# Kernel optimization log

Hardware: AMD Instinct MI355X
Metric: run time of the kernel (lower is better)

## Reference

```python
import jax, jax.numpy as jnp
import numpy as np
from jax import lax

# Model dims (mamba_ssm defaults: d_state=16, d_conv=4, expand=2, dt_rank=ceil(d_model/16))
V = 16384       # vocab_size
D = 1024        # embedding_dim / d_model
C_CLS = 128     # num_CLS_classes
D_INNER = 2 * D # expand * d_model = 2048
N = 16          # d_state
K = 4           # d_conv
DT_RANK = (D + 15) // 16  # 64
B, L = 4, 512


def setup_inputs() -> dict:
    key = jax.random.key(0)
    ks = jax.random.split(key, 12)
    s = 0.02
    tokens = jax.random.randint(ks[0], (B, L), 0, V, dtype=jnp.int64)
    embedding = jax.random.normal(ks[1], (V, D), jnp.float32) * s
    in_proj_w = jax.random.normal(ks[2], (2 * D_INNER, D), jnp.float32) * s
    conv_w = jax.random.normal(ks[3], (D_INNER, 1, K), jnp.float32) * 0.1
    conv_b = jnp.zeros((D_INNER,), jnp.float32)
    x_proj_w = jax.random.normal(ks[4], (DT_RANK + 2 * N, D_INNER), jnp.float32) * s
    dt_proj_w = jax.random.normal(ks[5], (D_INNER, DT_RANK), jnp.float32) * s
    dt_proj_b = jax.random.uniform(ks[6], (D_INNER,), jnp.float32, -4.0, -2.0)  # softplus -> small dt
    A_log = jnp.log(jnp.broadcast_to(jnp.arange(1, N + 1, dtype=jnp.float32), (D_INNER, N)))
    D_param = jnp.ones((D_INNER,), jnp.float32)
    out_proj_w = jax.random.normal(ks[7], (D, D_INNER), jnp.float32) * s
    recon_w = jax.random.normal(ks[8], (V, D), jnp.float32) * s
    cls_w = jax.random.normal(ks[9], (C_CLS, D), jnp.float32) * s
    return dict(tokens=tokens, embedding=embedding, in_proj_w=in_proj_w,
                conv_w=conv_w, conv_b=conv_b, x_proj_w=x_proj_w,
                dt_proj_w=dt_proj_w, dt_proj_b=dt_proj_b, A_log=A_log,
                D_param=D_param, out_proj_w=out_proj_w, recon_w=recon_w, cls_w=cls_w)


def _mamba(h, in_proj_w, conv_w, conv_b, x_proj_w, dt_proj_w, dt_proj_b, A_log, D_param, out_proj_w):
    # h: (B, L, D)
    xz = jnp.einsum('bld,ed->ble', h, in_proj_w)          # (B, L, 2*D_INNER)
    x, z = jnp.split(xz, 2, axis=-1)                      # each (B, L, D_INNER)
    # causal depthwise conv1d along L
    xt = jnp.swapaxes(x, 1, 2)                            # (B, D_INNER, L)
    xt = lax.conv_general_dilated(xt, conv_w, window_strides=(1,),
                                  padding=[(K - 1, 0)],
                                  feature_group_count=D_INNER,
                                  dimension_numbers=('NCH', 'OIH', 'NCH'))
    xt = xt + conv_b[None, :, None]
    x = jax.nn.silu(jnp.swapaxes(xt, 1, 2))               # (B, L, D_INNER)
    # input-dependent dt, B, C
    x_dbl = jnp.einsum('bld,ed->ble', x, x_proj_w)        # (B, L, DT_RANK+2N)
    dt, Bm, Cm = jnp.split(x_dbl, [DT_RANK, DT_RANK + N], axis=-1)
    delta = jax.nn.softplus(jnp.einsum('blr,dr->bld', dt, dt_proj_w) + dt_proj_b)  # (B,L,D_INNER)
    A = -jnp.exp(A_log)                                   # (D_INNER, N)
    dA = jnp.exp(delta[..., None] * A)                    # (B,L,D_INNER,N)
    dBx = delta[..., None] * Bm[:, :, None, :] * x[..., None]  # (B,L,D_INNER,N)
    # selective scan over time (sequential recurrence)
    dA_t = jnp.swapaxes(dA, 0, 1)                         # (L,B,D_INNER,N)
    dBx_t = jnp.swapaxes(dBx, 0, 1)
    C_t = jnp.swapaxes(Cm, 0, 1)                          # (L,B,N)
    def step(hc, inp):
        a, bx, c = inp
        hc = a * hc + bx                                  # (B,D_INNER,N)
        y = jnp.einsum('bdn,bn->bd', hc, c)
        return hc, y
    h0 = jnp.zeros((x.shape[0], D_INNER, N), x.dtype)
    _, ys = lax.scan(step, h0, (dA_t, dBx_t, C_t))
    y = jnp.swapaxes(ys, 0, 1) + x * D_param              # (B,L,D_INNER)
    y = y * jax.nn.silu(z)
    return jnp.einsum('ble,de->bld', y, out_proj_w)       # (B,L,D)


def reference(tokens, embedding, in_proj_w, conv_w, conv_b, x_proj_w,
              dt_proj_w, dt_proj_b, A_log, D_param, out_proj_w, recon_w, cls_w):
    h = embedding[tokens]                                 # (B,L,D)
    h = _mamba(h, in_proj_w, conv_w, conv_b, x_proj_w, dt_proj_w, dt_proj_b,
               A_log, D_param, out_proj_w)
    recon = jnp.einsum('bld,vd->blv', h, recon_w)         # (B,L,V)
    pooled = h.mean(axis=1)                               # mean CLS pooling assumption
    cls = jnp.einsum('bd,cd->bc', pooled, cls_w)          # (B,C_CLS)
    return (recon, cls)
```

## Files before the change

kernel.cpp:

```cpp
#include <hip/hip_runtime.h>
#include <hip/hip_bf16.h>
#include <stdint.h>

#define DIN    2048
#define MROWS  2048
#define LSEQ   512
#define NV     16384
#define DMODEL 1024
#define NC     8
#define CL     64

typedef __attribute__((ext_vector_type(8))) short bf16x8;
typedef __attribute__((ext_vector_type(4))) float f32x4;

__device__ __forceinline__ uint16_t f2bf(float f) {
  uint32_t u = __builtin_bit_cast(uint32_t, f);
  u += 0x7fffu + ((u >> 16) & 1u);
  return (uint16_t)(u >> 16);
}

__device__ __forceinline__ void gld_lds16(const uint16_t* g, uint16_t* l) {
  __builtin_amdgcn_global_load_lds(
      (const __attribute__((address_space(1))) void*)g,
      (__attribute__((address_space(3))) void*)l,
      16, 0, 0);
}

__global__ __launch_bounds__(256) void gemm_bf16_kernel(
    const uint16_t* __restrict__ A, const uint16_t* __restrict__ B,
    float* __restrict__ C, int M, int N, int K, int kchunk)
{
  __shared__ uint16_t As[128 * 32];
  __shared__ uint16_t Bs[128 * 32];
  const int tid  = threadIdx.x;
  const int wid  = tid >> 6;
  const int lane = tid & 63;
  const int bm = blockIdx.y * 128;
  const int bn = blockIdx.x * 128;
  const int k_beg = blockIdx.z * kchunk;
  float* Cout = C + (size_t)blockIdx.z * M * N;

  const int fr = lane & 15;
  const int fg = lane >> 4;
  const int wm = (wid >> 1) * 64;
  const int wn = (wid & 1) * 64;

  const int srow = wid * 32 + (lane >> 2);
  const int skof = (lane & 3) * 8;
  const uint16_t* Ag = A + (size_t)(bm + srow) * K + skof;
  const uint16_t* Bg = B + (size_t)(bn + srow) * K + skof;
  uint16_t* Al = As + wid * 1024;
  uint16_t* Bl = Bs + wid * 1024;

  f32x4 acc[4][4] = {};

  for (int k0 = 0; k0 < kchunk; k0 += 32) {
    const int kk = k_beg + k0;
    gld_lds16(Ag + kk, Al);
    gld_lds16(Ag + (size_t)16 * K + kk, Al + 512);
    gld_lds16(Bg + kk, Bl);
    gld_lds16(Bg + (size_t)16 * K + kk, Bl + 512);
    asm volatile("s_waitcnt vmcnt(0)" ::: "memory");
    __syncthreads();
    bf16x8 af[4], bfr[4];
#pragma unroll
    for (int i = 0; i < 4; ++i)
      af[i] = *(const bf16x8*)(As + (wm + i * 16 + fr) * 32 + fg * 8);
#pragma unroll
    for (int j = 0; j < 4; ++j)
      bfr[j] = *(const bf16x8*)(Bs + (wn + j * 16 + fr) * 32 + fg * 8);
#pragma unroll
    for (int i = 0; i < 4; ++i)
#pragma unroll
      for (int j = 0; j < 4; ++j)
        acc[i][j] = __builtin_amdgcn_mfma_f32_16x16x32_bf16(af[i], bfr[j], acc[i][j], 0, 0, 0);
    __syncthreads();
  }

#pragma unroll
  for (int i = 0; i < 4; ++i) {
    const int r0 = bm + wm + i * 16 + fg * 4;
#pragma unroll
    for (int j = 0; j < 4; ++j) {
      const int c0 = bn + wn + j * 16 + fr;
#pragma unroll
      for (int r = 0; r < 4; ++r)
        Cout[(size_t)(r0 + r) * N + c0] = acc[i][j][r];
    }
  }
}

__global__ __launch_bounds__(256) void reduce_slices_kernel(
    const float* __restrict__ in, float* __restrict__ out, int n, int S) {
  const int i = blockIdx.x * 256 + threadIdx.x;
  if (i >= n) return;
  float s = 0.f;
  for (int z = 0; z < S; ++z) s += in[i + (size_t)z * n];
  out[i] = s;
}

__global__ __launch_bounds__(256) void embed_kernel(
    const int* __restrict__ tok, const float* __restrict__ emb, uint16_t* __restrict__ out) {
  const int m = blockIdx.x;
  const int t = tok[m];
  const float4 v = ((const float4*)(emb + (size_t)t * DMODEL))[threadIdx.x];
  ((ushort4*)(out + (size_t)m * DMODEL))[threadIdx.x] =
      make_ushort4(f2bf(v.x), f2bf(v.y), f2bf(v.z), f2bf(v.w));
}

__global__ __launch_bounds__(256) void cvt_bf16_kernel(
    const float* __restrict__ in, uint16_t* __restrict__ out, int n4) {
  const int i = blockIdx.x * 256 + threadIdx.x;
  if (i >= n4) return;
  const float4 v = ((const float4*)in)[i];
  ((ushort4*)out)[i] = make_ushort4(f2bf(v.x), f2bf(v.y), f2bf(v.z), f2bf(v.w));
}

__global__ __launch_bounds__(256) void cvt_pad_kernel(
    const float* __restrict__ in, uint16_t* __restrict__ out, int rows_in, int cols4) {
  const int i = blockIdx.x * 256 + threadIdx.x;
  const int r = i / cols4, c = i % cols4;
  ushort4 o = make_ushort4(0, 0, 0, 0);
  if (r < rows_in) {
    const float4 v = ((const float4*)in)[(size_t)r * cols4 + c];
    o = make_ushort4(f2bf(v.x), f2bf(v.y), f2bf(v.z), f2bf(v.w));
  }
  ((ushort4*)out)[i] = o;
}

__global__ __launch_bounds__(256) void conv_silu_kernel(
    const float* __restrict__ xz, const float* __restrict__ cw, const float* __restrict__ cb,
    float* __restrict__ xc, uint16_t* __restrict__ xcb)
{
  const int idx = blockIdx.x * 256 + threadIdx.x;
  const int d = idx & (DIN - 1);
  const int m = idx >> 11;
  const int l = m & (LSEQ - 1);
  float acc = cb[d];
#pragma unroll
  for (int j = 0; j < 4; ++j) {
    const int lj = l - 3 + j;
    if (lj >= 0) acc += cw[d * 4 + j] * xz[(size_t)(m - 3 + j) * 4096 + d];
  }
  const float r = acc / (1.f + __expf(-acc));
  xc[idx] = r;
  xcb[idx] = f2bf(r);
}

__global__ __launch_bounds__(256) void dt_extract_kernel(
    const float* __restrict__ xdbl, uint16_t* __restrict__ dtb) {
  const int i = blockIdx.x * 256 + threadIdx.x;
  const int m = i >> 6, r = i & 63;
  dtb[i] = f2bf(xdbl[(size_t)m * 128 + r]);
}

__global__ __launch_bounds__(256) void softplus_kernel(
    float* __restrict__ dlt, const float* __restrict__ bias) {
  const int i = blockIdx.x * 256 + threadIdx.x;
  const int d = i & (DIN - 1);
  const float u = dlt[i] + bias[d];
  dlt[i] = (u > 20.f) ? u : log1pf(__expf(u));
}

__global__ __launch_bounds__(256) void scan_partial_kernel(
    const float* __restrict__ delta, const float* __restrict__ xc,
    const float* __restrict__ xdbl, const float* __restrict__ A_log,
    float* __restrict__ Pb, float* __restrict__ Qb)
{
  const int q = threadIdx.x & 3;
  const int d_idx = threadIdx.x >> 2;
  const int c = blockIdx.x;
  const int d = blockIdx.y * 64 + d_idx;
  const int b = blockIdx.z;
  float Arow[4];
#pragma unroll
  for (int n = 0; n < 4; ++n)
    Arow[n] = -expf(A_log[d * 16 + q * 4 + n]);
  float P[4] = {1.f, 1.f, 1.f, 1.f};
  float Q[4] = {0.f, 0.f, 0.f, 0.f};
  const int l0 = c * CL;
#pragma unroll 4
  for (int li = 0; li < CL; ++li) {
    const int m = b * LSEQ + l0 + li;
    const float de = delta[(size_t)m * DIN + d];
    const float xv = xc[(size_t)m * DIN + d];
    const float dx = de * xv;
    const float4 Bv = *(const float4*)(xdbl + (size_t)m * 128 + 64 + q * 4);
    const float bv[4] = {Bv.x, Bv.y, Bv.z, Bv.w};
#pragma unroll
    for (int n = 0; n < 4; ++n) {
      const float a = __expf(de * Arow[n]);
      P[n] *= a;
      Q[n] = a * Q[n] + dx * bv[n];
    }
  }
  const size_t o = ((size_t)(b * NC + c) * DIN + d) * 16 + q * 4;
  *(float4*)(Pb + o) = make_float4(P[0], P[1], P[2], P[3]);
  *(float4*)(Qb + o) = make_float4(Q[0], Q[1], Q[2], Q[3]);
}

__global__ __launch_bounds__(256) void scan_bounds_kernel(
    const float* __restrict__ Pb, const float* __restrict__ Qb, float* __restrict__ Hi)
{
  const int i = blockIdx.x * 256 + threadIdx.x;
  const int b = i >> 15;
  const int r = i & 32767;
  float h = 0.f;
#pragma unroll
  for (int c = 0; c < NC; ++c) {
    const size_t o = ((size_t)(b * NC + c) << 15) + r;
    Hi[o] = h;
    h = Pb[o] * h + Qb[o];
  }
}

__global__ __launch_bounds__(256) void scan_final_kernel(
    const float* __restrict__ delta, const float* __restrict__ xc,
    const float* __restrict__ xdbl, const float* __restrict__ xz,
    const float* __restrict__ A_log, const float* __restrict__ Dp,
    const float* __restrict__ Hi, uint16_t* __restrict__ yb)
{
  const int q = threadIdx.x & 3;
  const int d_idx = threadIdx.x >> 2;
  const int c = blockIdx.x;
  const int d = blockIdx.y * 64 + d_idx;
  const int b = blockIdx.z;
  float Arow[4];
#pragma unroll
  for (int n = 0; n < 4; ++n)
    Arow[n] = -expf(A_log[d * 16 + q * 4 + n]);
  const float dpd = Dp[d];
  const size_t o = ((size_t)(b * NC + c) * DIN + d) * 16 + q * 4;
  const float4 Hv = *(const float4*)(Hi + o);
  float h[4] = {Hv.x, Hv.y, Hv.z, Hv.w};
  const int l0 = c * CL;
#pragma unroll 2
  for (int li = 0; li < CL; ++li) {
    const int m = b * LSEQ + l0 + li;
    const float de = delta[(size_t)m * DIN + d];
    const float xv = xc[(size_t)m * DIN + d];
    const float dx = de * xv;
    const float4 Bv = *(const float4*)(xdbl + (size_t)m * 128 + 64 + q * 4);
    const float4 Cv = *(const float4*)(xdbl + (size_t)m * 128 + 80 + q * 4);
    const float bv[4] = {Bv.x, Bv.y, Bv.z, Bv.w};
    const float cv[4] = {Cv.x, Cv.y, Cv.z, Cv.w};
    float yp = 0.f;
#pragma unroll
    for (int n = 0; n < 4; ++n) {
      const float a = __expf(de * Arow[n]);
      h[n] = a * h[n] + dx * bv[n];
      yp += h[n] * cv[n];
    }
    yp += __shfl_xor(yp, 1);
    yp += __shfl_xor(yp, 2);
    if (q == 0) {
      const float z = xz[(size_t)m * 4096 + 2048 + d];
      const float sil = z / (1.f + __expf(-z));
      yb[(size_t)m * DIN + d] = f2bf((yp + xv * dpd) * sil);
    }
  }
}

__global__ __launch_bounds__(256) void pool_kernel(
    const float* __restrict__ h2, float* __restrict__ pooled) {
  const int b = blockIdx.x, t = threadIdx.x;
  const float4* base = (const float4*)(h2 + (size_t)b * LSEQ * DMODEL);
  float sx = 0, sy = 0, sz = 0, sw = 0;
  for (int l = 0; l < LSEQ; ++l) {
    const float4 v = base[l * (DMODEL / 4) + t];
    sx += v.x; sy += v.y; sz += v.z; sw += v.w;
  }
  const float inv = 1.f / LSEQ;
  ((float4*)pooled)[b * (DMODEL / 4) + t] = make_float4(sx * inv, sy * inv, sz * inv, sw * inv);
}

__global__ __launch_bounds__(64) void cls_kernel(
    const float* __restrict__ pooled, const float* __restrict__ w, float* __restrict__ out) {
  const int o = blockIdx.x;
  const int b = o >> 7, c = o & 127;
  const int lane = threadIdx.x;
  const float* p = pooled + b * 1024;
  const float* wr = w + c * 1024;
  float s = 0.f;
  for (int k = lane; k < 1024; k += 64) s += p[k] * wr[k];
#pragma unroll
  for (int off = 32; off > 0; off >>= 1) s += __shfl_down(s, off);
  if (lane == 0) out[o] = s;
}

extern "C" void kernel_launch(void* const* d_in, const int* in_sizes, int n_in,
                              void* d_out, int out_size, void* d_ws, size_t ws_size,
                              hipStream_t stream) {
  const int*   tokens    = (const int*)d_in[0];
  const float* embedding = (const float*)d_in[1];
  const float* in_proj_w = (const float*)d_in[2];
  const float* conv_w    = (const float*)d_in[3];
  const float* conv_b    = (const float*)d_in[4];
  const float* x_proj_w  = (const float*)d_in[5];
  const float* dt_proj_w = (const float*)d_in[6];
  const float* dt_proj_b = (const float*)d_in[7];
  const float* A_log     = (const float*)d_in[8];
  const float* D_param   = (const float*)d_in[9];
  const float* out_prj_w = (const float*)d_in[10];
  const float* recon_w   = (const float*)d_in[11];
  const float* cls_w     = (const float*)d_in[12];

  char* ws = (char*)d_ws;
  const size_t MB = 1024 * 1024;
  uint16_t* h_bf   = (uint16_t*)(ws + 0);
  uint16_t* w_in   = (uint16_t*)(ws + 4 * MB);
  float*    xz     = (float*)(ws + 12 * MB);
  float*    xc_f   = (float*)(ws + 44 * MB);
  uint16_t* xc_b   = (uint16_t*)(ws + 60 * MB);
  uint16_t* wx_bf  = (uint16_t*)(ws + 68 * MB);
  float*    xdbl   = (float*)(ws + 69 * MB);
  uint16_t* dt_bf  = (uint16_t*)(ws + 70 * MB);
  uint16_t* wdt_bf = (uint16_t*)(ws + 71 * MB);
  float*    delta  = (float*)(ws + 72 * MB);
  uint16_t* y_bf   = (uint16_t*)(ws + 88 * MB);
  uint16_t* h2_bf  = (uint16_t*)(ws + 96 * MB);
  float*    pooled = (float*)(ws + 100 * MB);
  uint16_t* wout_bf = h_bf;
  float*    h2_f    = (float*)w_in;
  uint16_t* wrec_bf = (uint16_t*)xz;
  float*    kscr    = delta;
  float*    Pbuf    = (float*)(ws + 60 * MB);
  float*    Qbuf    = (float*)(ws + 64 * MB);
  float*    Hinit   = (float*)(ws + 4 * MB);

  const int RECON = MROWS * NV;

  embed_kernel<<<dim3(MROWS), dim3(256), 0, stream>>>(tokens, embedding, h_bf);
  cvt_bf16_kernel<<<dim3(4096), dim3(256), 0, stream>>>(in_proj_w, w_in, 4096 * 1024 / 4);
  gemm_bf16_kernel<<<dim3(32, 16, 1), dim3(256), 0, stream>>>(h_bf, w_in, xz, MROWS, 4096, 1024, 1024);
  cvt_bf16_kernel<<<dim3(2048), dim3(256), 0, stream>>>(out_prj_w, wout_bf, 1024 * 2048 / 4);
  cvt_bf16_kernel<<<dim3(128), dim3(256), 0, stream>>>(dt_proj_w, wdt_bf, 2048 * 64 / 4);
  cvt_pad_kernel<<<dim3(256), dim3(256), 0, stream>>>(x_proj_w, wx_bf, 96, 512);
  conv_silu_kernel<<<dim3(16384), dim3(256), 0, stream>>>(xz, conv_w, conv_b, xc_f, xc_b);
  gemm_bf16_kernel<<<dim3(1, 16, 4), dim3(256), 0, stream>>>(xc_b, wx_bf, kscr, MROWS, 128, 2048, 512);
  reduce_slices_kernel<<<dim3(1024), dim3(256), 0, stream>>>(kscr, xdbl, MROWS * 128, 4);
  dt_extract_kernel<<<dim3(512), dim3(256), 0, stream>>>(xdbl, dt_bf);
  gemm_bf16_kernel<<<dim3(16, 16, 1), dim3(256), 0, stream>>>(dt_bf, wdt_bf, delta, MROWS, DIN, 64, 64);
  softplus_kernel<<<dim3(16384), dim3(256), 0, stream>>>(delta, dt_proj_b);
  scan_partial_kernel<<<dim3(NC, 32, 4), dim3(256), 0, stream>>>(delta, xc_f, xdbl, A_log, Pbuf, Qbuf);
  scan_bounds_kernel<<<dim3(512), dim3(256), 0, stream>>>(Pbuf, Qbuf, Hinit);
  scan_final_kernel<<<dim3(NC, 32, 4), dim3(256), 0, stream>>>(delta, xc_f, xdbl, xz, A_log, D_param, Hinit, y_bf);
  cvt_bf16_kernel<<<dim3(16384), dim3(256), 0, stream>>>(recon_w, wrec_bf, NV * 1024 / 4);
  gemm_bf16_kernel<<<dim3(8, 16, 2), dim3(256), 0, stream>>>(y_bf, wout_bf, kscr, MROWS, 1024, 2048, 1024);
  reduce_slices_kernel<<<dim3(8192), dim3(256), 0, stream>>>(kscr, h2_f, MROWS * 1024, 2);
  cvt_bf16_kernel<<<dim3(2048), dim3(256), 0, stream>>>(h2_f, h2_bf, MROWS * 1024 / 4);
  gemm_bf16_kernel<<<dim3(128, 16, 1), dim3(256), 0, stream>>>(h2_bf, wrec_bf, (float*)d_out, MROWS, NV, 1024, 1024);
  pool_kernel<<<dim3(4), dim3(256), 0, stream>>>(h2_f, pooled);
  cls_kernel<<<dim3(512), dim3(64), 0, stream>>>(pooled, cls_w, (float*)d_out + RECON);
}
```

Measured before the change: 386.4 us.

## Add 256x256-tile pipelined bf16 GEMM and use it for the large projections

Adds a new 512-thread GEMM kernel that computes 256x256 output tiles. It keeps a 4-stage LDS ring fed by direct global-to-LDS loads, uses XOR swizzling, s_setprio around the MFMAs, and an XCD-aware block swizzle. The kernel replaces the 128x128 GEMM for in_proj, out_proj and the recon projection. For out_proj it drops the split-K path and its reduce kernel. The larger tiles give more operand reuse and deeper prefetch. In exchange, out_proj gets only 32 workgroups, so occupancy is lower there, and register pressure is high with 128 accumulator values per thread.

```diff
diff --git a/kernel.cpp b/kernel.cpp
--- a/kernel.cpp
+++ b/kernel.cpp
@@ -24,6 +24,103 @@
       (const __attribute__((address_space(1))) void*)g,
       (__attribute__((address_space(3))) void*)l,
       16, 0, 0);
+}
+
+__global__ __launch_bounds__(512, 2) void gemm256_bf16_kernel(
+    const uint16_t* __restrict__ A, const uint16_t* __restrict__ B,
+    float* __restrict__ C, int M, int N, int K)
+{
+  __shared__ uint16_t lds[4 * 16384];
+  const int tid = threadIdx.x;
+  const int w   = tid >> 6;
+  const int l   = tid & 63;
+
+  const int nwg = gridDim.x;
+  const int cpx = nwg >> 3;
+  const int swz = (blockIdx.x & 7) * cpx + (blockIdx.x >> 3);
+  const int nmy = M >> 8;
+  const int bm  = (swz % nmy) << 8;
+  const int bn  = (swz / nmy) << 8;
+
+  const int fr = l & 15;
+  const int fg = l >> 4;
+  const int wr = w >> 2;
+  const int wc = w & 3;
+
+  const int srow = l >> 2;
+  const int kof  = (((l & 3) ^ ((l >> 3) & 3)) << 3);
+  const int ar0  = (w * 2 + 0) * 16 + srow;
+  const int ar1  = (w * 2 + 1) * 16 + srow;
+  const uint16_t* Ag0 = A + (size_t)(bm + ar0) * K + kof;
+  const uint16_t* Ag1 = A + (size_t)(bm + ar1) * K + kof;
+  const uint16_t* Bg0 = B + (size_t)(bn + ar0) * K + kof;
+  const uint16_t* Bg1 = B + (size_t)(bn + ar1) * K + kof;
+  const int lA0 = (w * 2 + 0) * 512;
+  const int lA1 = (w * 2 + 1) * 512;
+  const int lB0 = 8192 + (w * 2 + 0) * 512;
+  const int lB1 = 8192 + (w * 2 + 1) * 512;
+
+  const int axr  = ((fg ^ ((fr >> 1) & 3)) << 3);
+  const int aoff = (wr * 128 + fr) * 32 + axr;
+  const int boff = 8192 + (wc * 64 + fr) * 32 + axr;
+
+  f32x4 acc[8][4] = {};
+  const int NT = K >> 5;
+
+  auto stage = [&](int t) {
+    const int sb = (t & 3) << 14;
+    const int k0 = t << 5;
+    gld_lds16(Ag0 + k0, lds + sb + lA0);
+    gld_lds16(Ag1 + k0, lds + sb + lA1);
+    gld_lds16(Bg0 + k0, lds + sb + lB0);
+    gld_lds16(Bg1 + k0, lds + sb + lB1);
+  };
+  auto compute_tile = [&](int sb) {
+    bf16x8 af[8], bfr[4];
+#pragma unroll
+    for (int mi = 0; mi < 8; ++mi)
+      af[mi] = *(const bf16x8*)(lds + sb + aoff + mi * 512);
+#pragma unroll
+    for (int ni = 0; ni < 4; ++ni)
+      bfr[ni] = *(const bf16x8*)(lds + sb + boff + ni * 512);
+    __builtin_amdgcn_s_setprio(1);
+#pragma unroll
+    for (int mi = 0; mi < 8; ++mi)
+#pragma unroll
+      for (int ni = 0; ni < 4; ++ni)
+        acc[mi][ni] = __builtin_amdgcn_mfma_f32_16x16x32_bf16(af[mi], bfr[ni], acc[mi][ni], 0, 0, 0);
+    __builtin_amdgcn_s_setprio(0);
+  };
+
+  stage(0); stage(1); stage(2);
+  asm volatile("s_waitcnt vmcnt(8)" ::: "memory");
+  __builtin_amdgcn_s_barrier();
+
+  for (int t = 0; t < NT - 3; ++t) {
+    stage(t + 3);
+    compute_tile((t & 3) << 14);
+    asm volatile("s_waitcnt vmcnt(8)" ::: "memory");
+    __builtin_amdgcn_s_barrier();
+  }
+  compute_tile(((NT - 3) & 3) << 14);
+  asm volatile("s_waitcnt vmcnt(4)" ::: "memory");
+  __builtin_amdgcn_s_barrier();
+  compute_tile(((NT - 2) & 3) << 14);
+  asm volatile("s_waitcnt vmcnt(0)" ::: "memory");
+  __builtin_amdgcn_s_barrier();
+  compute_tile(((NT - 1) & 3) << 14);
+
+#pragma unroll
+  for (int mi = 0; mi < 8; ++mi) {
+    const int r0 = bm + wr * 128 + mi * 16 + fg * 4;
+#pragma unroll
+    for (int ni = 0; ni < 4; ++ni) {
+      const int c0 = bn + wc * 64 + ni * 16 + fr;
+#pragma unroll
+      for (int r = 0; r < 4; ++r)
+        C[(size_t)(r0 + r) * N + c0] = acc[mi][ni][r];
+    }
+  }
 }
 
 __global__ __launch_bounds__(256) void gemm_bf16_kernel(
@@ -332,7 +429,7 @@
 
   embed_kernel<<<dim3(MROWS), dim3(256), 0, stream>>>(tokens, embedding, h_bf);
   cvt_bf16_kernel<<<dim3(4096), dim3(256), 0, stream>>>(in_proj_w, w_in, 4096 * 1024 / 4);
-  gemm_bf16_kernel<<<dim3(32, 16, 1), dim3(256), 0, stream>>>(h_bf, w_in, xz, MROWS, 4096, 1024, 1024);
+  gemm256_bf16_kernel<<<dim3(128), dim3(512), 0, stream>>>(h_bf, w_in, xz, MROWS, 4096, 1024);
   cvt_bf16_kernel<<<dim3(2048), dim3(256), 0, stream>>>(out_prj_w, wout_bf, 1024 * 2048 / 4);
   cvt_bf16_kernel<<<dim3(128), dim3(256), 0, stream>>>(dt_proj_w, wdt_bf, 2048 * 64 / 4);
   cvt_pad_kernel<<<dim3(256), dim3(256), 0, stream>>>(x_proj_w, wx_bf, 96, 512);
@@ -346,10 +443,9 @@
   scan_bounds_kernel<<<dim3(512), dim3(256), 0, stream>>>(Pbuf, Qbuf, Hinit);
   scan_final_kernel<<<dim3(NC, 32, 4), dim3(256), 0, stream>>>(delta, xc_f, xdbl, xz, A_log, D_param, Hinit, y_bf);
   cvt_bf16_kernel<<<dim3(16384), dim3(256), 0, stream>>>(recon_w, wrec_bf, NV * 1024 / 4);
-  gemm_bf16_kernel<<<dim3(8, 16, 2), dim3(256), 0, stream>>>(y_bf, wout_bf, kscr, MROWS, 1024, 2048, 1024);
-  reduce_slices_kernel<<<dim3(8192), dim3(256), 0, stream>>>(kscr, h2_f, MROWS * 1024, 2);
+  gemm256_bf16_kernel<<<dim3(32), dim3(512), 0, stream>>>(y_bf, wout_bf, h2_f, MROWS, 1024, 2048);
   cvt_bf16_kernel<<<dim3(2048), dim3(256), 0, stream>>>(h2_f, h2_bf, MROWS * 1024 / 4);
-  gemm_bf16_kernel<<<dim3(128, 16, 1), dim3(256), 0, stream>>>(h2_bf, wrec_bf, (float*)d_out, MROWS, NV, 1024, 1024);
+  gemm256_bf16_kernel<<<dim3(512), dim3(512), 0, stream>>>(h2_bf, wrec_bf, (float*)d_out, MROWS, NV, 1024);
   pool_kernel<<<dim3(4), dim3(256), 0, stream>>>(h2_f, pooled);
   cls_kernel<<<dim3(512), dim3(64), 0, stream>>>(pooled, cls_w, (float*)d_out + RECON);
 }
```

Result: no change. 382.9 us (-0.9%).
